# Optimization experiments

Measured on AMD Instinct MI355X. Metric: run time of the kernel, lower is better.

The kernel has to match this reference:

```python
import jax, jax.numpy as jnp
import numpy as np

B, S, D = 16, 8192, 512
H, K, V = 8, 64, 64
EPS = 1e-12  # tf.math.l2_normalize epsilon


def setup_inputs() -> dict:
    key = jax.random.key(0)
    ks = jax.random.split(key, 12)
    s = 0.02
    return {
        "x": jax.random.normal(ks[0], (B, S, D), jnp.float32),
        "mask": jnp.ones((B, S), dtype=bool),
        "Wq_r": jax.random.normal(ks[1], (H, D, K), jnp.float32) * s,
        "bq_r": jnp.zeros((H, K), jnp.float32),
        "Wq_i": jax.random.normal(ks[2], (H, D, K), jnp.float32) * s,
        "bq_i": jnp.zeros((H, K), jnp.float32),
        "Wv": jax.random.normal(ks[3], (H, D, V), jnp.float32) * s,
        "bv": jnp.zeros((H, V), jnp.float32),
        "key_real": jax.random.normal(ks[4], (H, K), jnp.float32),
        "key_imag": jax.random.normal(ks[5], (H, K), jnp.float32),
        "Wf": jax.random.normal(ks[6], (H * V, D), jnp.float32) * s,
        "bf": jnp.zeros((D,), jnp.float32),
    }


def reference(x, mask, Wq_r, bq_r, Wq_i, bq_i, Wv, bv, key_real, key_imag, Wf, bf):
    m = mask.astype(x.dtype)  # [B,S]
    # all heads' query (complex: real/imag) and value projections in batched GEMMs
    qr = jnp.einsum('bsd,hdk->bshk', x, Wq_r) + bq_r  # [B,S,H,K]
    qi = jnp.einsum('bsd,hdk->bshk', x, Wq_i) + bq_i
    v = jnp.einsum('bsd,hdv->bshv', x, Wv) + bv       # [B,S,H,V]
    # complex l2_normalize along last axis: z / sqrt(sum |z|^2)
    qn = jnp.sqrt(jnp.maximum(jnp.sum(qr * qr + qi * qi, -1, keepdims=True), EPS))
    qr, qi = qr / qn, qi / qn
    kn = jnp.sqrt(jnp.maximum(jnp.sum(key_real**2 + key_imag**2, -1, keepdims=True), EPS))
    kr, ki = key_real / kn, key_imag / kn             # [H,K]
    # real part of non-conjugated complex dot product (operation='real')
    score = jnp.einsum('bshk,hk->bsh', qr, kr) - jnp.einsum('bshk,hk->bsh', qi, ki)
    score = score * m[:, :, None]                     # [B,S,H]
    pooled = jnp.einsum('bsh,bshv->bhv', score, v)    # masked weighted sum over S
    res = pooled.reshape(pooled.shape[0], -1)          # concat heads -> [B,H*V]
    return res @ Wf + bf                               # feedforward -> [B,D]
```

## Files before the change

### kernel.cpp

```cpp
#include <hip/hip_runtime.h>
#include <hip/hip_bf16.h>


#define CB 16
#define CS 8192
#define CD 512
#define CH 8
#define CK 64
#define NCOL 128
#define TM 64
#define EPSV 1e-12f

typedef __attribute__((ext_vector_type(8))) unsigned short us8;
typedef __attribute__((ext_vector_type(8))) __bf16 bf16x8;
typedef __attribute__((ext_vector_type(4))) float f32x4;

__device__ __forceinline__ unsigned short f2bf(float f) {
  __hip_bfloat16 h = __float2bfloat16(f);
  return *reinterpret_cast<unsigned short*>(&h);
}
__device__ __forceinline__ float bf2f(unsigned short u) {
  unsigned int x = ((unsigned int)u) << 16;
  return __uint_as_float(x);
}
__device__ __forceinline__ bf16x8 as_bf(us8 u) { return __builtin_bit_cast(bf16x8, u); }

__global__ void cap_prep(const float* __restrict__ Wq_r, const float* __restrict__ Wq_i,
                         const float* __restrict__ key_real, const float* __restrict__ key_imag,
                         const float* __restrict__ bq_r, const float* __restrict__ bq_i,
                         unsigned short* __restrict__ wbt, float* __restrict__ wvec,
                         float* __restrict__ bqc) {
  int blk = blockIdx.x, tid = threadIdx.x;
  if (blk < CH * NCOL) {
    int h = blk >> 7, c = blk & 127;
    const float* src = (c < CK) ? (Wq_r + (size_t)h * CD * CK + c)
                                : (Wq_i + (size_t)h * CD * CK + (c - CK));
    for (int d = tid; d < CD; d += 256)
      wbt[(size_t)blk * CD + d] = f2bf(src[(size_t)d * CK]);
  } else {
    int h = blk - CH * NCOL;
    __shared__ float knsh;
    if (tid < 64) {
      float a = key_real[h * CK + tid], b = key_imag[h * CK + tid];
      float t = a * a + b * b;
      #pragma unroll
      for (int off = 1; off < 64; off <<= 1) t += __shfl_xor(t, off);
      if (tid == 0) knsh = sqrtf(fmaxf(t, EPSV));
    }
    __syncthreads();
    if (tid < NCOL) {
      int c = tid;
      float kn = knsh;
      wvec[h * NCOL + c] = (c < CK) ? key_real[h * CK + c] / kn
                                    : -key_imag[h * CK + (c - CK)] / kn;
      bqc[h * NCOL + c] = (c < CK) ? bq_r[h * CK + c] : bq_i[h * CK + (c - CK)];
    }
  }
}

#define XL_BYTES (TM * CD * 2)
#define WL_BYTES (NCOL * 256 * 2)
#define SMEM_BYTES (XL_BYTES + WL_BYTES + 512 + 512 + 2048)

__global__ __launch_bounds__(512, 2) void cap_main(
    const float* __restrict__ x, const int* __restrict__ mask,
    const unsigned short* __restrict__ wbt, const float* __restrict__ wvec,
    const float* __restrict__ bqc, float* __restrict__ yws, float* __restrict__ ssum) {
  extern __shared__ char smem[];
  char* Xl = smem;
  char* Wl = smem + XL_BYTES;
  float* partn = (float*)(smem + XL_BYTES + WL_BYTES);
  float* partm = partn + 128;
  float* scoresA = partm + 128;

  const int tid = threadIdx.x;
  const int w = tid >> 6, l = tid & 63;
  const int blk = blockIdx.x;
  const int b = blk >> 7;
  const int s0 = (blk & 127) * TM;
  const float* xrow = x + ((size_t)(b * CS + s0)) * CD;

  #pragma unroll
  for (int i = 0; i < 8; ++i) {
    int id = i * 512 + tid;
    int row = id >> 6, cc = id & 63;
    const float* src = xrow + row * CD + cc * 8;
    float4 f0 = *(const float4*)(src);
    float4 f1 = *(const float4*)(src + 4);
    us8 v;
    v[0] = f2bf(f0.x); v[1] = f2bf(f0.y); v[2] = f2bf(f0.z); v[3] = f2bf(f0.w);
    v[4] = f2bf(f1.x); v[5] = f2bf(f1.y); v[6] = f2bf(f1.z); v[7] = f2bf(f1.w);
    int byte = row * 1024 + ((cc * 16) ^ ((row & 7) << 4));
    *(us8*)(Xl + byte) = v;
  }

  const int rw = (w & 3) * 16;
  const int cw = (w >> 2) * 64;
  const int lr = l & 15;
  const int lk = (l >> 4) * 8;

  #pragma unroll 1
  for (int h = 0; h < CH; ++h) {
    f32x4 acc[4];
    #pragma unroll
    for (int f = 0; f < 4; ++f) acc[f] = (f32x4){0.f, 0.f, 0.f, 0.f};

    #pragma unroll 1
    for (int kc = 0; kc < 2; ++kc) {
      __syncthreads();
      #pragma unroll
      for (int i = 0; i < 8; ++i) {
        int id = i * 512 + tid;
        int col = id >> 5, kch = id & 31;
        us8 v = *(const us8*)(wbt + (((size_t)(h * NCOL + col)) * CD + kc * 256 + kch * 8));
        int byte = col * 512 + ((kch * 16) ^ ((col & 7) << 4));
        *(us8*)(Wl + byte) = v;
      }
      __syncthreads();
      #pragma unroll
      for (int ks = 0; ks < 8; ++ks) {
        int kloc = ks * 32 + lk;
        int arow = rw + lr;
        int abyte = arow * 1024 + ((((kc * 256 + kloc)) * 2) ^ ((arow & 7) << 4));
        bf16x8 a = as_bf(*(const us8*)(Xl + abyte));
        #pragma unroll
        for (int f = 0; f < 4; ++f) {
          int col = cw + f * 16 + lr;
          int bbyte = col * 512 + ((kloc * 2) ^ ((col & 7) << 4));
          bf16x8 bb = as_bf(*(const us8*)(Wl + bbyte));
          acc[f] = __builtin_amdgcn_mfma_f32_16x16x32_bf16(a, bb, acc[f], 0, 0, 0);
        }
      }
    }

    float n2[4] = {0.f, 0.f, 0.f, 0.f}, nm[4] = {0.f, 0.f, 0.f, 0.f};
    #pragma unroll
    for (int f = 0; f < 4; ++f) {
      int c = cw + f * 16 + lr;
      float wv = wvec[h * NCOL + c];
      float bq = bqc[h * NCOL + c];
      #pragma unroll
      for (int r = 0; r < 4; ++r) {
        float q = acc[f][r] + bq;
        n2[r] += q * q;
        nm[r] += q * wv;
      }
    }
    #pragma unroll
    for (int off = 1; off < 16; off <<= 1) {
      #pragma unroll
      for (int r = 0; r < 4; ++r) {
        n2[r] += __shfl_xor(n2[r], off);
        nm[r] += __shfl_xor(nm[r], off);
      }
    }
    if (lr == 0) {
      int half = w >> 2;
      #pragma unroll
      for (int r = 0; r < 4; ++r) {
        int row = rw + (l >> 4) * 4 + r;
        partn[half * 64 + row] = n2[r];
        partm[half * 64 + row] = nm[r];
      }
    }
    __syncthreads();
    if (tid < 64) {
      float norm2 = partn[tid] + partn[64 + tid];
      float num = partm[tid] + partm[64 + tid];
      float qn = sqrtf(fmaxf(norm2, EPSV));
      float mk = (mask[(size_t)b * CS + s0 + tid] != 0) ? 1.0f : 0.0f;
      float sc = num / qn * mk;
      scoresA[h * 64 + tid] = sc;
      float t = sc;
      #pragma unroll
      for (int off = 1; off < 64; off <<= 1) t += __shfl_xor(t, off);
      if (tid == 0) atomicAdd(&ssum[b * CH + h], t);
    }
  }
  __syncthreads();

  {
    int d = tid;
    float sreg[CH];
    #pragma unroll
    for (int h = 0; h < CH; ++h) sreg[h] = scoresA[h * 64 + l];
    float yacc[CH];
    #pragma unroll
    for (int h = 0; h < CH; ++h) yacc[h] = 0.f;
    #pragma unroll 4
    for (int row = 0; row < TM; ++row) {
      int byte = row * 1024 + ((d * 2) ^ ((row & 7) << 4));
      float xv = bf2f(*(const unsigned short*)(Xl + byte));
      #pragma unroll
      for (int h = 0; h < CH; ++h) {
        float sc = __uint_as_float(
            __builtin_amdgcn_readlane(__float_as_uint(sreg[h]), row));
        yacc[h] += sc * xv;
      }
    }
    #pragma unroll
    for (int h = 0; h < CH; ++h)
      atomicAdd(&yws[((size_t)b * CH + h) * CD + d], yacc[h]);
  }
}

__global__ void cap_finish(const float* __restrict__ yws, const float* __restrict__ ssum,
                           const float* __restrict__ Wv, const float* __restrict__ bv,
                           const float* __restrict__ Wf, const float* __restrict__ bfv,
                           float* __restrict__ out) {
  __shared__ float yl[CH * CD];
  __shared__ float pl[CH * CK];
  __shared__ float ss[CH];
  int b = blockIdx.x, tid = threadIdx.x;
  for (int i = tid; i < CH * CD; i += 256) yl[i] = yws[(size_t)b * CH * CD + i];
  if (tid < CH) ss[tid] = ssum[b * CH + tid];
  __syncthreads();
  #pragma unroll
  for (int jj = 0; jj < 2; ++jj) {
    int j = jj * 256 + tid;
    int h = j >> 6, v = j & 63;
    float acc = ss[h] * bv[h * CK + v];
    const float* yrow = yl + h * CD;
    const float* wcol = Wv + (size_t)h * CD * CK + v;
    #pragma unroll 8
    for (int d = 0; d < CD; ++d) acc += yrow[d] * wcol[(size_t)d * CK];
    pl[j] = acc;
  }
  __syncthreads();
  #pragma unroll
  for (int jj = 0; jj < 2; ++jj) {
    int dout = jj * 256 + tid;
    float o = bfv[dout];
    #pragma unroll 8
    for (int j = 0; j < CH * CK; ++j) o += pl[j] * Wf[(size_t)j * CD + dout];
    out[b * CD + dout] = o;
  }
}

extern "C" void kernel_launch(void* const* d_in, const int* in_sizes, int n_in,
                              void* d_out, int out_size, void* d_ws, size_t ws_size,
                              hipStream_t stream) {
  const float* x = (const float*)d_in[0];
  const int* mask = (const int*)d_in[1];
  const float* Wq_r = (const float*)d_in[2];
  const float* bq_r = (const float*)d_in[3];
  const float* Wq_i = (const float*)d_in[4];
  const float* bq_i = (const float*)d_in[5];
  const float* Wv = (const float*)d_in[6];
  const float* bv = (const float*)d_in[7];
  const float* key_real = (const float*)d_in[8];
  const float* key_imag = (const float*)d_in[9];
  const float* Wf = (const float*)d_in[10];
  const float* bfv = (const float*)d_in[11];
  float* out = (float*)d_out;

  char* ws = (char*)d_ws;
  unsigned short* wbt = (unsigned short*)ws;
  float* wvec = (float*)(ws + (1 << 20));
  float* bqc = (float*)(ws + (1 << 20) + 4096);
  float* yws = (float*)(ws + (1 << 20) + 8192);
  float* ssum = (float*)(ws + (1 << 20) + 8192 + CB * CH * CD * 4);

  hipMemsetAsync(yws, 0, CB * CH * CD * 4 + CB * CH * 4, stream);
  cap_prep<<<dim3(CH * NCOL + CH), dim3(256), 0, stream>>>(
      Wq_r, Wq_i, key_real, key_imag, bq_r, bq_i, wbt, wvec, bqc);
  hipFuncSetAttribute((const void*)cap_main,
                      hipFuncAttributeMaxDynamicSharedMemorySize, SMEM_BYTES);
  cap_main<<<dim3(CB * (CS / TM)), dim3(512), SMEM_BYTES, stream>>>(
      x, mask, wbt, wvec, bqc, yws, ssum);
  cap_finish<<<dim3(CB), dim3(256), 0, stream>>>(yws, ssum, Wv, bv, Wf, bfv, out);
}
```

Before: 889.2 us.

## Restructure main GEMM with 4-head column tiles, double-buffered async W loads, split finish

The main kernel now computes 512 query columns (four heads) per pass with a 4x4 MFMA register tile per wave, so each A fragment is reused across more columns. W tiles are streamed into LDS through double-buffered global_load_lds, overlapping the copy with MFMA work. The weight transpose prep now goes through an LDS tile to get coalesced accesses. The single-block-per-batch finish kernel is split into two wider kernels that parallelise the Wv and Wf products. Register pressure rises under a 512-thread, 2-block launch bound, and the kernel count grows.

```diff
diff --git a/kernel.cpp b/kernel.cpp
--- a/kernel.cpp
+++ b/kernel.cpp
@@ -25,42 +25,53 @@
 }
 __device__ __forceinline__ bf16x8 as_bf(us8 u) { return __builtin_bit_cast(bf16x8, u); }
 
+#define G2L16(gp, lp)                                                  \
+  __builtin_amdgcn_global_load_lds(                                    \
+      (const __attribute__((address_space(1))) unsigned int*)(gp),     \
+      (__attribute__((address_space(3))) unsigned int*)(lp), 16, 0, 0)
+
 __global__ void cap_prep(const float* __restrict__ Wq_r, const float* __restrict__ Wq_i,
-                         const float* __restrict__ key_real, const float* __restrict__ key_imag,
+                         unsigned short* __restrict__ wbt) {
+  __shared__ float tile[64][65];
+  int blk = blockIdx.x, t = threadIdx.x;
+  int ri = blk >> 6, h = (blk >> 3) & 7, dt = blk & 7;
+  const float* src = (ri ? Wq_i : Wq_r) + (size_t)h * CD * CK + (size_t)dt * 64 * CK;
+  #pragma unroll
+  for (int p = 0; p < 16; ++p) {
+    int idx = p * 256 + t;
+    int d = idx >> 6, c = idx & 63;
+    tile[d][c] = src[(size_t)d * CK + c];
+  }
+  __syncthreads();
+  int l = t & 63;
+  #pragma unroll
+  for (int p = 0; p < 16; ++p) {
+    int c = p * 4 + (t >> 6);
+    wbt[((size_t)(h * NCOL + ri * 64 + c)) * CD + dt * 64 + l] = f2bf(tile[l][c]);
+  }
+}
+
+__global__ void cap_keys(const float* __restrict__ key_real, const float* __restrict__ key_imag,
                          const float* __restrict__ bq_r, const float* __restrict__ bq_i,
-                         unsigned short* __restrict__ wbt, float* __restrict__ wvec,
-                         float* __restrict__ bqc) {
-  int blk = blockIdx.x, tid = threadIdx.x;
-  if (blk < CH * NCOL) {
-    int h = blk >> 7, c = blk & 127;
-    const float* src = (c < CK) ? (Wq_r + (size_t)h * CD * CK + c)
-                                : (Wq_i + (size_t)h * CD * CK + (c - CK));
-    for (int d = tid; d < CD; d += 256)
-      wbt[(size_t)blk * CD + d] = f2bf(src[(size_t)d * CK]);
-  } else {
-    int h = blk - CH * NCOL;
-    __shared__ float knsh;
-    if (tid < 64) {
-      float a = key_real[h * CK + tid], b = key_imag[h * CK + tid];
-      float t = a * a + b * b;
-      #pragma unroll
-      for (int off = 1; off < 64; off <<= 1) t += __shfl_xor(t, off);
-      if (tid == 0) knsh = sqrtf(fmaxf(t, EPSV));
-    }
-    __syncthreads();
-    if (tid < NCOL) {
-      int c = tid;
-      float kn = knsh;
-      wvec[h * NCOL + c] = (c < CK) ? key_real[h * CK + c] / kn
-                                    : -key_imag[h * CK + (c - CK)] / kn;
-      bqc[h * NCOL + c] = (c < CK) ? bq_r[h * CK + c] : bq_i[h * CK + (c - CK)];
-    }
-  }
-}
-
-#define XL_BYTES (TM * CD * 2)
-#define WL_BYTES (NCOL * 256 * 2)
-#define SMEM_BYTES (XL_BYTES + WL_BYTES + 512 + 512 + 2048)
+                         float* __restrict__ wvec, float* __restrict__ bqc) {
+  int h = blockIdx.x, t = threadIdx.x;
+  __shared__ float kn;
+  if (t < 64) {
+    float a = key_real[h * CK + t], b2 = key_imag[h * CK + t];
+    float s = a * a + b2 * b2;
+    #pragma unroll
+    for (int off = 1; off < 64; off <<= 1) s += __shfl_xor(s, off);
+    if (t == 0) kn = sqrtf(fmaxf(s, EPSV));
+  }
+  __syncthreads();
+  float v = (t < CK) ? key_real[h * CK + t] : -key_imag[h * CK + (t - CK)];
+  wvec[h * NCOL + t] = v / kn;
+  bqc[h * NCOL + t] = (t < CK) ? bq_r[h * CK + t] : bq_i[h * CK + (t - CK)];
+}
+
+#define XL_BYTES 65536
+#define WBUF_BYTES 32768
+#define SMEM_BYTES (XL_BYTES + 2 * WBUF_BYTES + 3 * 2048)
 
 __global__ __launch_bounds__(512, 2) void cap_main(
     const float* __restrict__ x, const int* __restrict__ mask,
@@ -68,17 +79,34 @@
     const float* __restrict__ bqc, float* __restrict__ yws, float* __restrict__ ssum) {
   extern __shared__ char smem[];
   char* Xl = smem;
-  char* Wl = smem + XL_BYTES;
-  float* partn = (float*)(smem + XL_BYTES + WL_BYTES);
-  float* partm = partn + 128;
-  float* scoresA = partm + 128;
+  char* Wb = smem + XL_BYTES;
+  float* partn = (float*)(smem + XL_BYTES + 2 * WBUF_BYTES);
+  float* partm = partn + 512;
+  float* scoresA = partm + 512;
 
   const int tid = threadIdx.x;
   const int w = tid >> 6, l = tid & 63;
-  const int blk = blockIdx.x;
-  const int b = blk >> 7;
-  const int s0 = (blk & 127) * TM;
+  const int lr = l & 15, q = l >> 4;
+  const int b = blockIdx.x >> 7;
+  const int s0 = (blockIdx.x & 127) * TM;
   const float* xrow = x + ((size_t)(b * CS + s0)) * CD;
+
+  auto stageW = [&](int s) {
+    if (s >= 32) return;
+    int ch = s >> 4, kc = s & 15;
+    char* dst = Wb + (size_t)(s & 1) * WBUF_BYTES;
+    #pragma unroll
+    for (int i = 0; i < 4; ++i) {
+      int o = i * 8192 + tid * 16;
+      int col_local = o >> 6;
+      int kchunk = (o >> 4) & 3;
+      const unsigned short* src =
+          wbt + ((size_t)(ch * 512 + col_local)) * CD + kc * 32 + kchunk * 8;
+      G2L16(src, dst + o);
+    }
+  };
+
+  stageW(0);
 
   #pragma unroll
   for (int i = 0; i < 8; ++i) {
@@ -93,91 +121,99 @@
     int byte = row * 1024 + ((cc * 16) ^ ((row & 7) << 4));
     *(us8*)(Xl + byte) = v;
   }
-
-  const int rw = (w & 3) * 16;
-  const int cw = (w >> 2) * 64;
-  const int lr = l & 15;
-  const int lk = (l >> 4) * 8;
+  __syncthreads();
 
   #pragma unroll 1
-  for (int h = 0; h < CH; ++h) {
-    f32x4 acc[4];
-    #pragma unroll
-    for (int f = 0; f < 4; ++f) acc[f] = (f32x4){0.f, 0.f, 0.f, 0.f};
+  for (int ch = 0; ch < 2; ++ch) {
+    f32x4 acc[4][4];
+    #pragma unroll
+    for (int m = 0; m < 4; ++m)
+      #pragma unroll
+      for (int n = 0; n < 4; ++n) acc[m][n] = (f32x4){0.f, 0.f, 0.f, 0.f};
 
     #pragma unroll 1
-    for (int kc = 0; kc < 2; ++kc) {
+    for (int kc = 0; kc < 16; ++kc) {
+      int gp = ch * 16 + kc;
+      stageW(gp + 1);
+      char* wl = Wb + (size_t)(gp & 1) * WBUF_BYTES;
+      int kbyte = kc * 64 + q * 16;
+      bf16x8 a[4], bb[4];
+      #pragma unroll
+      for (int m = 0; m < 4; ++m) {
+        int row = m * 16 + lr;
+        a[m] = as_bf(*(const us8*)(Xl + row * 1024 + (kbyte ^ ((row & 7) << 4))));
+      }
+      #pragma unroll
+      for (int n = 0; n < 4; ++n) {
+        int col_local = w * 64 + n * 16 + lr;
+        bb[n] = as_bf(*(const us8*)(wl + col_local * 64 + q * 16));
+      }
+      #pragma unroll
+      for (int m = 0; m < 4; ++m)
+        #pragma unroll
+        for (int n = 0; n < 4; ++n)
+          acc[m][n] = __builtin_amdgcn_mfma_f32_16x16x32_bf16(a[m], bb[n], acc[m][n], 0, 0, 0);
       __syncthreads();
-      #pragma unroll
-      for (int i = 0; i < 8; ++i) {
-        int id = i * 512 + tid;
-        int col = id >> 5, kch = id & 31;
-        us8 v = *(const us8*)(wbt + (((size_t)(h * NCOL + col)) * CD + kc * 256 + kch * 8));
-        int byte = col * 512 + ((kch * 16) ^ ((col & 7) << 4));
-        *(us8*)(Wl + byte) = v;
+    }
+
+    {
+      int h = ch * 4 + (w >> 1);
+      float n2[4][4], nm[4][4];
+      #pragma unroll
+      for (int m = 0; m < 4; ++m)
+        #pragma unroll
+        for (int r = 0; r < 4; ++r) { n2[m][r] = 0.f; nm[m][r] = 0.f; }
+      #pragma unroll
+      for (int n = 0; n < 4; ++n) {
+        int c = (w & 1) * 64 + n * 16 + lr;
+        float wv = wvec[h * NCOL + c];
+        float bq = bqc[h * NCOL + c];
+        #pragma unroll
+        for (int m = 0; m < 4; ++m)
+          #pragma unroll
+          for (int r = 0; r < 4; ++r) {
+            float qv = acc[m][n][r] + bq;
+            n2[m][r] += qv * qv;
+            nm[m][r] += qv * wv;
+          }
+      }
+      #pragma unroll
+      for (int off = 1; off < 16; off <<= 1)
+        #pragma unroll
+        for (int m = 0; m < 4; ++m)
+          #pragma unroll
+          for (int r = 0; r < 4; ++r) {
+            n2[m][r] += __shfl_xor(n2[m][r], off);
+            nm[m][r] += __shfl_xor(nm[m][r], off);
+          }
+      if (lr == 0) {
+        #pragma unroll
+        for (int m = 0; m < 4; ++m)
+          #pragma unroll
+          for (int r = 0; r < 4; ++r) {
+            int row = m * 16 + q * 4 + r;
+            partn[w * 64 + row] = n2[m][r];
+            partm[w * 64 + row] = nm[m][r];
+          }
       }
       __syncthreads();
-      #pragma unroll
-      for (int ks = 0; ks < 8; ++ks) {
-        int kloc = ks * 32 + lk;
-        int arow = rw + lr;
-        int abyte = arow * 1024 + ((((kc * 256 + kloc)) * 2) ^ ((arow & 7) << 4));
-        bf16x8 a = as_bf(*(const us8*)(Xl + abyte));
-        #pragma unroll
-        for (int f = 0; f < 4; ++f) {
-          int col = cw + f * 16 + lr;
-          int bbyte = col * 512 + ((kloc * 2) ^ ((col & 7) << 4));
-          bf16x8 bb = as_bf(*(const us8*)(Wl + bbyte));
-          acc[f] = __builtin_amdgcn_mfma_f32_16x16x32_bf16(a, bb, acc[f], 0, 0, 0);
+      if (tid < 64) {
+        float mk = (mask[(size_t)b * CS + s0 + tid] != 0) ? 1.0f : 0.0f;
+        #pragma unroll
+        for (int hl = 0; hl < 4; ++hl) {
+          float nn = partn[(2 * hl) * 64 + tid] + partn[(2 * hl + 1) * 64 + tid];
+          float mm = partm[(2 * hl) * 64 + tid] + partm[(2 * hl + 1) * 64 + tid];
+          float sc = mm / sqrtf(fmaxf(nn, EPSV)) * mk;
+          scoresA[(ch * 4 + hl) * 64 + tid] = sc;
+          float ts = sc;
+          #pragma unroll
+          for (int off = 1; off < 64; off <<= 1) ts += __shfl_xor(ts, off);
+          if (tid == 0) atomicAdd(&ssum[b * CH + ch * 4 + hl], ts);
         }
       }
+      __syncthreads();
     }
-
-    float n2[4] = {0.f, 0.f, 0.f, 0.f}, nm[4] = {0.f, 0.f, 0.f, 0.f};
-    #pragma unroll
-    for (int f = 0; f < 4; ++f) {
-      int c = cw + f * 16 + lr;
-      float wv = wvec[h * NCOL + c];
-      float bq = bqc[h * NCOL + c];
-      #pragma unroll
-      for (int r = 0; r < 4; ++r) {
-        float q = acc[f][r] + bq;
-        n2[r] += q * q;
-        nm[r] += q * wv;
-      }
-    }
-    #pragma unroll
-    for (int off = 1; off < 16; off <<= 1) {
-      #pragma unroll
-      for (int r = 0; r < 4; ++r) {
-        n2[r] += __shfl_xor(n2[r], off);
-        nm[r] += __shfl_xor(nm[r], off);
-      }
-    }
-    if (lr == 0) {
-      int half = w >> 2;
-      #pragma unroll
-      for (int r = 0; r < 4; ++r) {
-        int row = rw + (l >> 4) * 4 + r;
-        partn[half * 64 + row] = n2[r];
-        partm[half * 64 + row] = nm[r];
-      }
-    }
-    __syncthreads();
-    if (tid < 64) {
-      float norm2 = partn[tid] + partn[64 + tid];
-      float num = partm[tid] + partm[64 + tid];
-      float qn = sqrtf(fmaxf(norm2, EPSV));
-      float mk = (mask[(size_t)b * CS + s0 + tid] != 0) ? 1.0f : 0.0f;
-      float sc = num / qn * mk;
-      scoresA[h * 64 + tid] = sc;
-      float t = sc;
-      #pragma unroll
-      for (int off = 1; off < 64; off <<= 1) t += __shfl_xor(t, off);
-      if (tid == 0) atomicAdd(&ssum[b * CH + h], t);
-    }
-  }
-  __syncthreads();
+  }
 
   {
     int d = tid;
@@ -204,37 +240,49 @@
   }
 }
 
-__global__ void cap_finish(const float* __restrict__ yws, const float* __restrict__ ssum,
+__global__ void cap_pooled(const float* __restrict__ yws, const float* __restrict__ ssum,
                            const float* __restrict__ Wv, const float* __restrict__ bv,
-                           const float* __restrict__ Wf, const float* __restrict__ bfv,
-                           float* __restrict__ out) {
-  __shared__ float yl[CH * CD];
-  __shared__ float pl[CH * CK];
-  __shared__ float ss[CH];
-  int b = blockIdx.x, tid = threadIdx.x;
-  for (int i = tid; i < CH * CD; i += 256) yl[i] = yws[(size_t)b * CH * CD + i];
-  if (tid < CH) ss[tid] = ssum[b * CH + tid];
-  __syncthreads();
-  #pragma unroll
-  for (int jj = 0; jj < 2; ++jj) {
-    int j = jj * 256 + tid;
-    int h = j >> 6, v = j & 63;
-    float acc = ss[h] * bv[h * CK + v];
-    const float* yrow = yl + h * CD;
-    const float* wcol = Wv + (size_t)h * CD * CK + v;
-    #pragma unroll 8
-    for (int d = 0; d < CD; ++d) acc += yrow[d] * wcol[(size_t)d * CK];
-    pl[j] = acc;
-  }
-  __syncthreads();
-  #pragma unroll
-  for (int jj = 0; jj < 2; ++jj) {
-    int dout = jj * 256 + tid;
-    float o = bfv[dout];
-    #pragma unroll 8
-    for (int j = 0; j < CH * CK; ++j) o += pl[j] * Wf[(size_t)j * CD + dout];
-    out[b * CD + dout] = o;
-  }
+                           float* __restrict__ pooled) {
+  int blk = blockIdx.x, t = threadIdx.x;
+  int b = blk >> 3, h = blk & 7;
+  int v = t & 63, dq = t >> 6;
+  const float* y = yws + ((size_t)b * CH + h) * CD;
+  const float* wv = Wv + (size_t)h * CD * CK;
+  float acc = 0.f;
+  #pragma unroll 8
+  for (int i = 0; i < 128; ++i) {
+    int d = i * 4 + dq;
+    acc += y[d] * wv[(size_t)d * CK + v];
+  }
+  __shared__ float red[4][64];
+  red[dq][v] = acc;
+  __syncthreads();
+  if (t < 64) {
+    float s = red[0][t] + red[1][t] + red[2][t] + red[3][t] +
+              ssum[b * CH + h] * bv[h * CK + t];
+    pooled[(size_t)b * 512 + h * 64 + t] = s;
+  }
+}
+
+__global__ void cap_out(const float* __restrict__ pooled, const float* __restrict__ Wf,
+                        const float* __restrict__ bfv, float* __restrict__ out) {
+  int blk = blockIdx.x, t = threadIdx.x;
+  int b = blk >> 3, dc = blk & 7;
+  int dl = t & 63, jq = t >> 6;
+  int dout = dc * 64 + dl;
+  const float* pr = pooled + (size_t)b * 512;
+  float acc = 0.f;
+  #pragma unroll 8
+  for (int i = 0; i < 128; ++i) {
+    int j = i * 4 + jq;
+    acc += pr[j] * Wf[(size_t)j * CD + dout];
+  }
+  __shared__ float red[4][64];
+  red[jq][dl] = acc;
+  __syncthreads();
+  if (t < 64)
+    out[(size_t)b * CD + dc * 64 + t] =
+        red[0][t] + red[1][t] + red[2][t] + red[3][t] + bfv[dc * 64 + t];
 }
 
 extern "C" void kernel_launch(void* const* d_in, const int* in_sizes, int n_in,
@@ -257,16 +305,18 @@
   char* ws = (char*)d_ws;
   unsigned short* wbt = (unsigned short*)ws;
   float* wvec = (float*)(ws + (1 << 20));
-  float* bqc = (float*)(ws + (1 << 20) + 4096);
-  float* yws = (float*)(ws + (1 << 20) + 8192);
+  float* bqc  = (float*)(ws + (1 << 20) + 4096);
+  float* yws  = (float*)(ws + (1 << 20) + 8192);
   float* ssum = (float*)(ws + (1 << 20) + 8192 + CB * CH * CD * 4);
+  float* pooled = (float*)(ws + (1 << 20) + 8192 + CB * CH * CD * 4 + 512);
 
   hipMemsetAsync(yws, 0, CB * CH * CD * 4 + CB * CH * 4, stream);
-  cap_prep<<<dim3(CH * NCOL + CH), dim3(256), 0, stream>>>(
-      Wq_r, Wq_i, key_real, key_imag, bq_r, bq_i, wbt, wvec, bqc);
+  cap_prep<<<dim3(128), dim3(256), 0, stream>>>(Wq_r, Wq_i, wbt);
+  cap_keys<<<dim3(8), dim3(128), 0, stream>>>(key_real, key_imag, bq_r, bq_i, wvec, bqc);
   hipFuncSetAttribute((const void*)cap_main,
                       hipFuncAttributeMaxDynamicSharedMemorySize, SMEM_BYTES);
   cap_main<<<dim3(CB * (CS / TM)), dim3(512), SMEM_BYTES, stream>>>(
       x, mask, wbt, wvec, bqc, yws, ssum);
-  cap_finish<<<dim3(CB), dim3(256), 0, stream>>>(yws, ssum, Wv, bv, Wf, bfv, out);
-}
+  cap_pooled<<<dim3(128), dim3(256), 0, stream>>>(yws, ssum, Wv, bv, pooled);
+  cap_out<<<dim3(128), dim3(256), 0, stream>>>(pooled, Wf, bfv, out);
+}
```

After: 735.1 us. -17.3%, faster.
